# Performance work log

Measured on AMD Instinct MI355X. Metric: run time of the kernel, lower is better.

The kernel has to match this reference:

```python
import jax, jax.numpy as jnp
import numpy as np

D = 512       # d_model
M = 64        # working memory_dim
SE = 32       # episodic slots
SS = 64       # semantic slots
H = 4         # episodic heads
B, L = 2, 1024
BOT = max(D // 4, 32)  # controller bottleneck = 128


def _layernorm(x, g, b, eps=1e-5):
    mu = jnp.mean(x, axis=-1, keepdims=True)
    var = jnp.var(x, axis=-1, keepdims=True)
    return (x - mu) * jax.lax.rsqrt(var + eps) * g + b


def setup_inputs() -> dict:
    key = jax.random.key(0)
    ks = jax.random.split(key, 24)
    r = lambda i, shape, s=0.02: jax.random.normal(ks[i], shape, dtype=jnp.float32) * s
    return {
        "x": jax.random.normal(ks[0], (B, L, D), dtype=jnp.float32),
        # WorkingMemory (weights stored as (in, out))
        "Wq": r(1, (D, M)), "Wk": r(2, (D, M)), "Wv": r(3, (D, D)),
        "Wf": r(4, (D, M)), "bf": jnp.zeros((M,), jnp.float32),
        "Wo": r(5, (D, D)),
        "ln_g": jnp.ones((D,), jnp.float32), "ln_b": jnp.zeros((D,), jnp.float32),
        # EpisodicMemory
        "eslots": r(6, (1, SE, D)),
        "Eq": r(7, (D, D)), "Ek": r(8, (D, D)), "Ev": r(9, (D, D)), "Eo": r(10, (D, D)),
        # SemanticMemory
        "know": r(11, (1, SS, D)),
        "Sin": r(12, (D, D)),
        "Sg_w": r(13, (D, D)), "Sg_b": jnp.zeros((D,), jnp.float32),
        "So": r(14, (D, D)),
        # MemoryController
        "C1w": r(15, (D, BOT)), "C1b": jnp.zeros((BOT,), jnp.float32),
        "C2w": r(16, (BOT, 3)), "C2b": jnp.zeros((3,), jnp.float32),
    }


def _forward(x, Wq, Wk, Wv, Wf, bf, Wo, ln_g, ln_b,
             eslots, Eq, Ek, Ev, Eo,
             know, Sin, Sg_w, Sg_b, So,
             C1w, C1b, C2w, C2b):
    b, l, d = x.shape
    # ---- WorkingMemory (parallel gated linear attention) ----
    scale = M ** -0.5
    q = (jax.nn.elu(x @ Wq) + 1.0) * scale          # (B,L,M)
    k = jax.nn.elu(x @ Wk) + 1.0                    # (B,L,M)
    v = x @ Wv                                      # (B,L,D)
    forget = jax.nn.sigmoid(x @ Wf + bf)            # (B,L,M)
    log_f_cum = jnp.clip(jnp.cumsum(jnp.log(jnp.clip(forget, 1e-6, None)), axis=1), -20.0, 20.0)
    exp_neg = jnp.exp(-log_f_cum)
    exp_pos = jnp.exp(log_f_cum)
    kv = k[..., :, None] * v[..., None, :]          # (B,L,M,D) outer product
    cum_kv = jnp.cumsum(exp_neg[..., None] * kv, axis=1)
    Mstate = exp_pos[..., None] * cum_kv            # (B,L,M,D)
    z = exp_pos * jnp.cumsum(exp_neg * k, axis=1)   # (B,L,M)
    num = jnp.einsum('blm,blmd->bld', q, Mstate)
    den = jnp.einsum('blm,blm->bl', q, z)[..., None] + 1e-6
    w_out = _layernorm(num / den, ln_g, ln_b) @ Wo  # (B,L,D)

    # ---- EpisodicMemory (cross-attn to learned slots) ----
    hd = D // H
    mem = jnp.broadcast_to(eslots, (b, SE, D))
    qh = (x @ Eq).reshape(b, l, H, hd)
    kh = (mem @ Ek).reshape(b, SE, H, hd)
    vh = (mem @ Ev).reshape(b, SE, H, hd)
    scores = jnp.einsum('blhe,bshe->bhls', qh, kh) / jnp.sqrt(jnp.float32(hd))
    attn = jax.nn.softmax(scores, axis=-1)
    e_out = jnp.einsum('bhls,bshe->blhe', attn, vh).reshape(b, l, D) @ Eo

    # ---- SemanticMemory (single-head attn to knowledge, gated residual) ----
    kb = jnp.broadcast_to(know, (b, SS, D))
    qs = x @ Sin                                    # (B,L,D)
    s_scores = jnp.einsum('bld,bsd->bls', qs, kb) / jnp.sqrt(jnp.float32(D))
    s_attn = jax.nn.softmax(s_scores, axis=-1)
    retrieved = jnp.einsum('bls,bsd->bld', s_attn, kb)
    gate = jax.nn.sigmoid(x @ Sg_w + Sg_b)
    s_out = (gate * retrieved + (1.0 - gate) * x) @ So

    # ---- Controller fusion ----
    wts = jax.nn.softmax(jax.nn.silu(x @ C1w + C1b) @ C2w + C2b, axis=-1)  # (B,L,3)
    fused = (wts[..., 0:1] * w_out + wts[..., 1:2] * e_out + wts[..., 2:3] * s_out)
    return fused


def reference(x, Wq, Wk, Wv, Wf, bf, Wo, ln_g, ln_b,
              eslots, Eq, Ek, Ev, Eo,
              know, Sin, Sg_w, Sg_b, So,
              C1w, C1b, C2w, C2b):
    return _forward(x, Wq, Wk, Wv, Wf, bf, Wo, ln_g, ln_b,
                    eslots, Eq, Ek, Ev, Eo,
                    know, Sin, Sg_w, Sg_b, So,
                    C1w, C1b, C2w, C2b)
```

## Files before the change

kernel.cpp:

```cpp
#include <hip/hip_runtime.h>
#include <cstdint>

typedef unsigned int uint;
typedef unsigned short ushort;
typedef __attribute__((ext_vector_type(8))) short bf16x8;
typedef __attribute__((ext_vector_type(4))) float f32x4;

__device__ __forceinline__ ushort f2b(float f) {
  union { float f; uint u; } v; v.f = f;
  uint u = v.u;
  uint r = (u + 0x7FFFu + ((u >> 16) & 1u)) >> 16;
  return (ushort)r;
}
__device__ __forceinline__ float b2f(ushort h) {
  union { uint u; float f; } v; v.u = ((uint)h) << 16; return v.f;
}

__global__ __launch_bounds__(256) void k_prep(
    const float* __restrict__ x, const float* __restrict__ Wv, const float* __restrict__ Sg,
    const float* __restrict__ C1w, const float* __restrict__ Wq, const float* __restrict__ Wk,
    const float* __restrict__ Wo, const float* __restrict__ So, const float* __restrict__ know,
    const float* __restrict__ eslots, const float* __restrict__ Ek, const float* __restrict__ Ev,
    const float* __restrict__ Sin, const float* __restrict__ Wf, const float* __restrict__ bfb,
    ushort* __restrict__ X16, ushort* __restrict__ Wcat, ushort* __restrict__ Wfin,
    ushort* __restrict__ know16, float* __restrict__ kh, float* __restrict__ vh,
    float* __restrict__ logfb)
{
  __shared__ __align__(16) float Af[16 * 32];
  __shared__ __align__(16) float Bf[32 * 64];
  __shared__ __align__(16) float T[64][65];
  int bid = blockIdx.x;
  int tid = threadIdx.x;
  int lane = tid & 63, wv = tid >> 6;

  if (bid < 128) {
    int r0 = bid * 16;
    int row = tid >> 4, col4 = (tid & 15) * 4;
    float a0 = 0.f, a1 = 0.f, a2 = 0.f, a3 = 0.f;
    for (int kt = 0; kt < 16; ++kt) {
      if (tid < 128) {
        int p = tid; int rr = p >> 3, c4 = (p & 7) * 4;
        *(float4*)&Af[rr * 32 + c4] = *(const float4*)&x[(size_t)(r0 + rr) * 512 + kt * 32 + c4];
      }
      #pragma unroll
      for (int i = 0; i < 2; ++i) {
        int p = i * 256 + tid; int rr = p >> 4, c4 = (p & 15) * 4;
        *(float4*)&Bf[rr * 64 + c4] = *(const float4*)&Wf[(size_t)(kt * 32 + rr) * 64 + c4];
      }
      __syncthreads();
      #pragma unroll 8
      for (int ks = 0; ks < 32; ++ks) {
        float a = Af[row * 32 + ks];
        float4 b = *(float4*)&Bf[ks * 64 + col4];
        a0 += a * b.x; a1 += a * b.y; a2 += a * b.z; a3 += a * b.w;
      }
      __syncthreads();
    }
    float accs[4] = {a0, a1, a2, a3};
    #pragma unroll
    for (int j = 0; j < 4; ++j) {
      float logit = accs[j] + bfb[col4 + j];
      float s = 1.f / (1.f + expf(-logit));
      logfb[(size_t)(r0 + row) * 64 + col4 + j] = logf(fmaxf(s, 1e-6f));
    }
    return;
  }
  if (bid < 256) {
    int t = (bid - 128) * 256 + tid;
    if (t < 16384) {
      int s = t >> 9, j = t & 511;
      float acc = 0.f;
      #pragma unroll 8
      for (int d = 0; d < 512; ++d) acc += eslots[s * 512 + d] * Ek[d * 512 + j];
      kh[s * 512 + j] = acc;
    } else {
      int o = t - 16384; int s = o >> 9, j = o & 511;
      float acc = 0.f;
      #pragma unroll 8
      for (int d = 0; d < 512; ++d) acc += eslots[s * 512 + d] * Ev[d * 512 + j];
      vh[s * 512 + j] = acc;
    }
    return;
  }
  if (bid < 384) {
    int k = (bid - 256) * 4 + wv;
    const float* sp = Sin + (size_t)k * 512 + lane * 8;
    float4 s1 = *(const float4*)&sp[0];
    float4 s2 = *(const float4*)&sp[4];
    for (int s = 0; s < 64; ++s) {
      const float* kp = know + (size_t)s * 512 + lane * 8;
      float4 k1 = *(const float4*)&kp[0];
      float4 k2 = *(const float4*)&kp[4];
      float part = s1.x * k1.x + s1.y * k1.y + s1.z * k1.z + s1.w * k1.w
                 + s2.x * k2.x + s2.y * k2.y + s2.z * k2.z + s2.w * k2.w;
      #pragma unroll
      for (int o = 32; o; o >>= 1) part += __shfl_xor(part, o);
      if (lane == 0) Wcat[(640 + s) * 512 + k] = f2b(part * 0.04419417382415922f);
    }
    return;
  }
  if (bid < 672) {
    int tt = bid - 384;
    const float* src; ushort* dst; int sld, dld, Nt, drow, dcol;
    if (tt < 64)       {           src = Wv;  dst = Wcat; sld = 512; dld = 512;  Nt = 8; drow = 0;    dcol = 0;   }
    else if (tt < 128) { tt -= 64; src = Sg;  dst = Wcat; sld = 512; dld = 512;  Nt = 8; drow = 704;  dcol = 0;   }
    else if (tt < 144) { tt -= 128; src = C1w; dst = Wcat; sld = 128; dld = 512; Nt = 2; drow = 1216; dcol = 0;   }
    else if (tt < 152) { tt -= 144; src = Wq;  dst = Wcat; sld = 64;  dld = 512; Nt = 1; drow = 1344; dcol = 0;   }
    else if (tt < 160) { tt -= 152; src = Wk;  dst = Wcat; sld = 64;  dld = 512; Nt = 1; drow = 1408; dcol = 0;   }
    else if (tt < 224) { tt -= 160; src = Wo;  dst = Wfin; sld = 512; dld = 1152; Nt = 8; drow = 0;   dcol = 0;   }
    else               { tt -= 224; src = So;  dst = Wfin; sld = 512; dld = 1152; Nt = 8; drow = 0;   dcol = 512; }
    int tk = tt / Nt, tn = tt % Nt;
    int k0 = tk * 64, n0 = tn * 64;
    int r = tid >> 4, c = (tid & 15) * 4;
    #pragma unroll
    for (int p = 0; p < 4; ++p) {
      int kk = p * 16 + r;
      float4 v = *(const float4*)&src[(size_t)(k0 + kk) * sld + n0 + c];
      T[c + 0][kk] = v.x; T[c + 1][kk] = v.y; T[c + 2][kk] = v.z; T[c + 3][kk] = v.w;
    }
    __syncthreads();
    int n = tid >> 2, kc = (tid & 3) * 16;
    uint u[8];
    #pragma unroll
    for (int j = 0; j < 8; ++j) {
      ushort lo = f2b(T[n][kc + 2 * j]);
      ushort hi = f2b(T[n][kc + 2 * j + 1]);
      u[j] = (uint)lo | ((uint)hi << 16);
    }
    size_t off = (size_t)(drow + n0 + n) * dld + dcol + k0 + kc;
    uint4 o1; o1.x = u[0]; o1.y = u[1]; o1.z = u[2]; o1.w = u[3];
    uint4 o2; o2.x = u[4]; o2.y = u[5]; o2.z = u[6]; o2.w = u[7];
    *(uint4*)&dst[off] = o1;
    *(uint4*)&dst[off + 8] = o2;
    return;
  }
  if (bid < 800) {
    int base = (bid - 672) * 256 + tid;
    #pragma unroll
    for (int it = 0; it < 8; ++it) {
      int t = base + it * 32768;
      float4 xv = *(const float4*)&x[(size_t)t * 4];
      uint2 o;
      o.x = (uint)f2b(xv.x) | ((uint)f2b(xv.y) << 16);
      o.y = (uint)f2b(xv.z) | ((uint)f2b(xv.w) << 16);
      *(uint2*)&X16[(size_t)t * 4] = o;
    }
    return;
  }
  {
    int t = (bid - 800) * 256 + tid;
    #pragma unroll
    for (int j = 0; j < 2; ++j) {
      float4 v = *(const float4*)&know[(size_t)t * 8 + j * 4];
      uint2 o;
      o.x = (uint)f2b(v.x) | ((uint)f2b(v.y) << 16);
      o.y = (uint)f2b(v.z) | ((uint)f2b(v.w) << 16);
      *(uint2*)&know16[(size_t)t * 8 + j * 4] = o;
    }
  }
}

__global__ __launch_bounds__(256) void k_pre2(
    const float* __restrict__ Eq, const float* __restrict__ kh, const float* __restrict__ vh,
    const float* __restrict__ Eo, ushort* __restrict__ Wcat, ushort* __restrict__ Wfin)
{
  int bid = blockIdx.x;
  int tid = threadIdx.x;
  int lane = tid & 63, wv = tid >> 6;
  if (bid < 256) {
    int gw = bid * 4 + wv;
    #pragma unroll
    for (int pp = 0; pp < 2; ++pp) {
      int pair = gw * 2 + pp;
      int k = pair >> 2, h = pair & 3;
      const float* ep = Eq + (size_t)k * 512 + h * 128 + lane * 2;
      float e0 = ep[0], e1 = ep[1];
      for (int s = 0; s < 32; ++s) {
        const float* kp = kh + (size_t)s * 512 + h * 128 + lane * 2;
        float part = e0 * kp[0] + e1 * kp[1];
        #pragma unroll
        for (int o = 32; o; o >>= 1) part += __shfl_xor(part, o);
        if (lane == 0) Wcat[(512 + h * 32 + s) * 512 + k] = f2b(part * 0.08838834764831845f);
      }
    }
  } else {
    int o = (bid - 256) * 256 + tid;
    int hs = o >> 9, j = o & 511;
    int h = hs >> 5, s = hs & 31;
    const float* vhp = vh + (size_t)s * 512 + h * 128;
    float acc = 0.f;
    #pragma unroll 8
    for (int e = 0; e < 128; ++e) acc += vhp[e] * Eo[(size_t)(h * 128 + e) * 512 + j];
    Wfin[(size_t)j * 1152 + 1024 + hs] = f2b(acc);
  }
}

__global__ __launch_bounds__(256) void k_gemm1(
    const ushort* __restrict__ A, const ushort* __restrict__ Bw, float* __restrict__ C,
    const float* __restrict__ sgb, const float* __restrict__ c1b)
{
  __shared__ __align__(16) ushort As[64 * 32];
  __shared__ __align__(16) ushort Bs[128 * 32];
  int tid = threadIdx.x;
  int lane = tid & 63, wv = tid >> 6;
  int wm = (wv & 1) * 32, wn = (wv >> 1) * 64;
  int lr = lane & 15, lk = lane >> 4;
  int m0 = blockIdx.y * 64, n0 = blockIdx.x * 128;
  f32x4 zero4 = {0.f, 0.f, 0.f, 0.f};
  f32x4 acc[2][4];
  #pragma unroll
  for (int a = 0; a < 2; ++a)
    #pragma unroll
    for (int b = 0; b < 4; ++b) acc[a][b] = zero4;
  for (int kt = 0; kt < 16; ++kt) {
    int k0 = kt * 32;
    {
      int p = tid, row = p >> 2, cc = p & 3;
      int cs = cc ^ ((row >> 1) & 3);
      *(uint4*)&As[p * 8] = *(const uint4*)&A[(size_t)(m0 + row) * 512 + k0 + cs * 8];
    }
    #pragma unroll
    for (int i = 0; i < 2; ++i) {
      int p = i * 256 + tid, row = p >> 2, cc = p & 3;
      int cs = cc ^ ((row >> 1) & 3);
      *(uint4*)&Bs[p * 8] = *(const uint4*)&Bw[(size_t)(n0 + row) * 512 + k0 + cs * 8];
    }
    __syncthreads();
    bf16x8 af[2], bfv[4];
    #pragma unroll
    for (int mi = 0; mi < 2; ++mi) {
      int row = wm + mi * 16 + lr;
      int cc = lk ^ ((row >> 1) & 3);
      af[mi] = *(bf16x8*)&As[row * 32 + cc * 8];
    }
    #pragma unroll
    for (int ni = 0; ni < 4; ++ni) {
      int row = wn + ni * 16 + lr;
      int cc = lk ^ ((row >> 1) & 3);
      bfv[ni] = *(bf16x8*)&Bs[row * 32 + cc * 8];
    }
    #pragma unroll
    for (int mi = 0; mi < 2; ++mi)
      #pragma unroll
      for (int ni = 0; ni < 4; ++ni)
        acc[mi][ni] = __builtin_amdgcn_mfma_f32_16x16x32_bf16(af[mi], bfv[ni], acc[mi][ni], 0, 0, 0);
    __syncthreads();
  }
  #pragma unroll
  for (int mi = 0; mi < 2; ++mi) {
    #pragma unroll
    for (int ni = 0; ni < 4; ++ni) {
      int col = n0 + wn + ni * 16 + lr;
      #pragma unroll
      for (int r = 0; r < 4; ++r) {
        int rowb = m0 + wm + mi * 16 + lk * 4 + r;
        float v = acc[mi][ni][r];
        if (col >= 704) {
          if (col < 1216) { v = 1.f / (1.f + __expf(-(v + sgb[col - 704]))); }
          else if (col < 1344) { float tt = v + c1b[col - 1216]; v = tt / (1.f + __expf(-tt)); }
          else if (col < 1408) { float e = (v > 0.f) ? v : (__expf(v) - 1.f); v = (e + 1.f) * 0.125f; }
          else if (col < 1472) { float e = (v > 0.f) ? v : (__expf(v) - 1.f); v = e + 1.f; }
        }
        C[(size_t)rowb * 1536 + col] = v;
      }
    }
  }
}

__global__ __launch_bounds__(256) void k_gemm2(
    const ushort* __restrict__ A, const ushort* __restrict__ Bw, float* __restrict__ C)
{
  __shared__ __align__(16) ushort As[64 * 32];
  __shared__ __align__(16) ushort Bs[64 * 32];
  int tid = threadIdx.x;
  int lane = tid & 63, wv = tid >> 6;
  int wm = (wv & 1) * 32, wn = (wv >> 1) * 32;
  int lr = lane & 15, lk = lane >> 4;
  int m0 = blockIdx.y * 64, n0 = blockIdx.x * 64;
  f32x4 zero4 = {0.f, 0.f, 0.f, 0.f};
  f32x4 acc[2][2];
  #pragma unroll
  for (int a = 0; a < 2; ++a)
    #pragma unroll
    for (int b = 0; b < 2; ++b) acc[a][b] = zero4;
  for (int kt = 0; kt < 36; ++kt) {
    int k0 = kt * 32;
    {
      int p = tid, row = p >> 2, cc = p & 3;
      int cs = cc ^ ((row >> 1) & 3);
      *(uint4*)&As[p * 8] = *(const uint4*)&A[(size_t)(m0 + row) * 1152 + k0 + cs * 8];
      *(uint4*)&Bs[p * 8] = *(const uint4*)&Bw[(size_t)(n0 + row) * 1152 + k0 + cs * 8];
    }
    __syncthreads();
    bf16x8 af[2], bfv[2];
    #pragma unroll
    for (int mi = 0; mi < 2; ++mi) {
      int row = wm + mi * 16 + lr;
      int cc = lk ^ ((row >> 1) & 3);
      af[mi] = *(bf16x8*)&As[row * 32 + cc * 8];
    }
    #pragma unroll
    for (int ni = 0; ni < 2; ++ni) {
      int row = wn + ni * 16 + lr;
      int cc = lk ^ ((row >> 1) & 3);
      bfv[ni] = *(bf16x8*)&Bs[row * 32 + cc * 8];
    }
    #pragma unroll
    for (int mi = 0; mi < 2; ++mi)
      #pragma unroll
      for (int ni = 0; ni < 2; ++ni)
        acc[mi][ni] = __builtin_amdgcn_mfma_f32_16x16x32_bf16(af[mi], bfv[ni], acc[mi][ni], 0, 0, 0);
    __syncthreads();
  }
  #pragma unroll
  for (int mi = 0; mi < 2; ++mi) {
    #pragma unroll
    for (int ni = 0; ni < 2; ++ni) {
      int col = n0 + wn + ni * 16 + lr;
      #pragma unroll
      for (int r = 0; r < 4; ++r) {
        int rowb = m0 + wm + mi * 16 + lk * 4 + r;
        C[(size_t)rowb * 512 + col] = acc[mi][ni][r];
      }
    }
  }
}

__global__ __launch_bounds__(256) void k_gatescan(
    const float* __restrict__ logfb, const float* __restrict__ P,
    float* __restrict__ cn, float* __restrict__ qe, float* __restrict__ qz)
{
  __shared__ float wsumA[4];
  __shared__ float wsumB[4];
  int bidx = blockIdx.x;
  int b = bidx >> 6, m = bidx & 63;
  int tid = threadIdx.x;
  int lane = tid & 63, wv = tid >> 6;
  size_t rbase = (size_t)b * 1024 + tid * 4;

  float v0 = logfb[(rbase + 0) * 64 + m];
  float v1 = logfb[(rbase + 1) * 64 + m];
  float v2 = logfb[(rbase + 2) * 64 + m];
  float v3 = logfb[(rbase + 3) * 64 + m];
  v1 += v0; v2 += v1; v3 += v2;
  float tsum = v3;
  float sc = tsum;
  #pragma unroll
  for (int o = 1; o < 64; o <<= 1) {
    float t = __shfl_up(sc, o, 64);
    if (lane >= o) sc += t;
  }
  if (lane == 63) wsumA[wv] = sc;
  __syncthreads();
  float excl = sc - tsum;
  #pragma unroll
  for (int w2 = 0; w2 < 3; ++w2) if (w2 < wv) excl += wsumA[w2];

  float vv[4] = {v0, v1, v2, v3};
  float cv[4], qv[4];
  #pragma unroll
  for (int i = 0; i < 4; ++i) {
    size_t r = rbase + i;
    float lf = fminf(fmaxf(excl + vv[i], -20.f), 20.f);
    float en = expf(-lf), ep = expf(lf);
    float kk = P[r * 1536 + 1408 + m];
    float qq = P[r * 1536 + 1344 + m];
    cv[i] = en * kk;
    qv[i] = qq * ep;
    cn[r * 64 + m] = cv[i];
    qe[r * 64 + m] = qv[i];
  }

  float c1 = cv[0], c2 = c1 + cv[1], c3 = c2 + cv[2], c4 = c3 + cv[3];
  float t2 = c4;
  float sc2 = t2;
  #pragma unroll
  for (int o = 1; o < 64; o <<= 1) {
    float t = __shfl_up(sc2, o, 64);
    if (lane >= o) sc2 += t;
  }
  if (lane == 63) wsumB[wv] = sc2;
  __syncthreads();
  float excl2 = sc2 - t2;
  #pragma unroll
  for (int w2 = 0; w2 < 3; ++w2) if (w2 < wv) excl2 += wsumB[w2];

  float pr[4] = {c1, c2, c3, c4};
  #pragma unroll
  for (int i = 0; i < 4; ++i) {
    size_t r = rbase + i;
    qz[r * 64 + m] = qv[i] * (excl2 + pr[i]);
  }
}

__global__ __launch_bounds__(256) void k_scanA(
    const float* __restrict__ cn, const float* __restrict__ P, float* __restrict__ Send)
{
  __shared__ __align__(16) float cnS[16 * 64];
  __shared__ __align__(16) float vS[16 * 64];
  int tid = threadIdx.x;
  int bid = blockIdx.x;
  int dt = bid & 7, c = (bid >> 3) & 15, b = bid >> 7;
  int rb0 = b * 1024 + c * 64;
  int mg = tid >> 4, dl = tid & 15;
  float4 acc[4];
  #pragma unroll
  for (int i = 0; i < 4; ++i) acc[i] = make_float4(0.f, 0.f, 0.f, 0.f);
  for (int ig = 0; ig < 4; ++ig) {
    int rb = rb0 + ig * 16;
    int row = tid >> 4, c4f = (tid & 15) * 4;
    *(float4*)&cnS[row * 64 + c4f] = *(const float4*)&cn[(size_t)(rb + row) * 64 + c4f];
    *(float4*)&vS[row * 64 + c4f] = *(const float4*)&P[(size_t)(rb + row) * 1536 + dt * 64 + c4f];
    __syncthreads();
    #pragma unroll 4
    for (int i = 0; i < 16; ++i) {
      float4 vv = *(float4*)&vS[i * 64 + dl * 4];
      float4 cm = *(float4*)&cnS[i * 64 + mg * 4];
      acc[0].x += cm.x * vv.x; acc[0].y += cm.x * vv.y; acc[0].z += cm.x * vv.z; acc[0].w += cm.x * vv.w;
      acc[1].x += cm.y * vv.x; acc[1].y += cm.y * vv.y; acc[1].z += cm.y * vv.z; acc[1].w += cm.y * vv.w;
      acc[2].x += cm.z * vv.x; acc[2].y += cm.z * vv.y; acc[2].z += cm.z * vv.z; acc[2].w += cm.z * vv.w;
      acc[3].x += cm.w * vv.x; acc[3].y += cm.w * vv.y; acc[3].z += cm.w * vv.z; acc[3].w += cm.w * vv.w;
    }
    __syncthreads();
  }
  #pragma unroll
  for (int mi = 0; mi < 4; ++mi) {
    int m = mg * 4 + mi;
    *(float4*)&Send[(size_t)((b * 16 + c) * 64 + m) * 512 + dt * 64 + dl * 4] = acc[mi];
  }
}

__global__ __launch_bounds__(256) void k_scanB(const float* __restrict__ Send, float* __restrict__ carry)
{
  int t = blockIdx.x * 256 + threadIdx.x;
  int d = t & 511, m = (t >> 9) & 63, b = t >> 15;
  float run = 0.f;
  for (int c = 0; c < 16; ++c) {
    size_t idx = (size_t)((b * 16 + c) * 64 + m) * 512 + d;
    carry[idx] = run;
    run += Send[idx];
  }
}

__global__ __launch_bounds__(256) void k_scanC(
    const float* __restrict__ cn, const float* __restrict__ qe, const float* __restrict__ P,
    const float* __restrict__ carry, float* __restrict__ num)
{
  __shared__ __align__(16) float cnS[16 * 64];
  __shared__ __align__(16) float qeS[16 * 64];
  __shared__ __align__(16) float vS[16 * 64];
  int tid = threadIdx.x;
  int bid = blockIdx.x;
  int dt = bid & 7, c = (bid >> 3) & 15, b = bid >> 7;
  int rb0 = b * 1024 + c * 64;
  int mg = tid & 3, dl = tid >> 2;
  int d = dt * 64 + dl;
  float S[16];
  #pragma unroll
  for (int mi = 0; mi < 16; ++mi)
    S[mi] = carry[(size_t)((b * 16 + c) * 64 + mg * 16 + mi) * 512 + d];
  for (int ig = 0; ig < 4; ++ig) {
    int rb = rb0 + ig * 16;
    int row = tid >> 4, c4f = (tid & 15) * 4;
    *(float4*)&cnS[row * 64 + c4f] = *(const float4*)&cn[(size_t)(rb + row) * 64 + c4f];
    *(float4*)&qeS[row * 64 + c4f] = *(const float4*)&qe[(size_t)(rb + row) * 64 + c4f];
    *(float4*)&vS[row * 64 + c4f] = *(const float4*)&P[(size_t)(rb + row) * 1536 + dt * 64 + c4f];
    __syncthreads();
    for (int i = 0; i < 16; ++i) {
      float vv = vS[i * 64 + dl];
      float p = 0.f;
      #pragma unroll
      for (int j = 0; j < 4; ++j) {
        float4 c4 = *(float4*)&cnS[i * 64 + mg * 16 + j * 4];
        float4 q4 = *(float4*)&qeS[i * 64 + mg * 16 + j * 4];
        S[j * 4 + 0] += c4.x * vv; p += q4.x * S[j * 4 + 0];
        S[j * 4 + 1] += c4.y * vv; p += q4.y * S[j * 4 + 1];
        S[j * 4 + 2] += c4.z * vv; p += q4.z * S[j * 4 + 2];
        S[j * 4 + 3] += c4.w * vv; p += q4.w * S[j * 4 + 3];
      }
      p += __shfl_xor(p, 1);
      p += __shfl_xor(p, 2);
      if (mg == 0) num[(size_t)(rb + i) * 512 + d] = p;
    }
    __syncthreads();
  }
}

__global__ __launch_bounds__(256) void k_post(
    const float* __restrict__ P, const float* __restrict__ x,
    const float* __restrict__ num, const float* __restrict__ qz,
    const ushort* __restrict__ know16, const float* __restrict__ lng,
    const float* __restrict__ lnb, const float* __restrict__ C2w,
    const float* __restrict__ C2b, ushort* __restrict__ Afin)
{
  __shared__ __align__(16) ushort kbuf[32 * 512];
  __shared__ float attnL[4][64];
  __shared__ float w2L[4];
  int tid = threadIdx.x;
  int w = tid >> 6, lane = tid & 63;
  int r0 = blockIdx.x * 4;
  int r = r0 + w;
  size_t pr = (size_t)r * 1536;

  float h0 = P[pr + 1216 + lane], h1 = P[pr + 1280 + lane];
  float a0 = h0 * C2w[lane * 3 + 0] + h1 * C2w[(64 + lane) * 3 + 0];
  float a1 = h0 * C2w[lane * 3 + 1] + h1 * C2w[(64 + lane) * 3 + 1];
  float a2 = h0 * C2w[lane * 3 + 2] + h1 * C2w[(64 + lane) * 3 + 2];
  #pragma unroll
  for (int o = 32; o; o >>= 1) {
    a0 += __shfl_xor(a0, o); a1 += __shfl_xor(a1, o); a2 += __shfl_xor(a2, o);
  }
  a0 += C2b[0]; a1 += C2b[1]; a2 += C2b[2];
  float mxc = fmaxf(a0, fmaxf(a1, a2));
  float e0 = expf(a0 - mxc), e1 = expf(a1 - mxc), e2c = expf(a2 - mxc);
  float inv = 1.f / (e0 + e1 + e2c);
  float w0 = e0 * inv, w1 = e1 * inv, w2 = e2c * inv;
  if (lane == 0) w2L[w] = w2;

  {
    float den = qz[(size_t)r * 64 + lane];
    #pragma unroll
    for (int o = 32; o; o >>= 1) den += __shfl_xor(den, o);
    den += 1e-6f;
    float y[8];
    float4 n0 = *(const float4*)&num[(size_t)r * 512 + lane * 8];
    float4 n1 = *(const float4*)&num[(size_t)r * 512 + lane * 8 + 4];
    y[0] = n0.x / den; y[1] = n0.y / den; y[2] = n0.z / den; y[3] = n0.w / den;
    y[4] = n1.x / den; y[5] = n1.y / den; y[6] = n1.z / den; y[7] = n1.w / den;
    float s1 = 0.f, s2 = 0.f;
    #pragma unroll
    for (int i = 0; i < 8; ++i) { s1 += y[i]; s2 += y[i] * y[i]; }
    #pragma unroll
    for (int o = 32; o; o >>= 1) { s1 += __shfl_xor(s1, o); s2 += __shfl_xor(s2, o); }
    float mu = s1 * (1.f / 512.f);
    float var = s2 * (1.f / 512.f) - mu * mu;
    float rs = rsqrtf(var + 1e-5f);
    uint4 outv;
    uint pk[4];
    #pragma unroll
    for (int p2 = 0; p2 < 4; ++p2) {
      float o0 = (y[2 * p2] - mu) * rs * lng[lane * 8 + 2 * p2] + lnb[lane * 8 + 2 * p2];
      float o1 = (y[2 * p2 + 1] - mu) * rs * lng[lane * 8 + 2 * p2 + 1] + lnb[lane * 8 + 2 * p2 + 1];
      pk[p2] = (uint)f2b(o0 * w0) | ((uint)f2b(o1 * w0) << 16);
    }
    outv.x = pk[0]; outv.y = pk[1]; outv.z = pk[2]; outv.w = pk[3];
    *(uint4*)&Afin[(size_t)r * 1152 + lane * 8] = outv;
  }

  {
    int h = lane >> 4, ei = (lane & 15) * 2;
    float v0 = P[pr + 512 + h * 32 + ei], v1 = P[pr + 512 + h * 32 + ei + 1];
    float mxe = fmaxf(v0, v1);
    #pragma unroll
    for (int o = 1; o < 16; o <<= 1) mxe = fmaxf(mxe, __shfl_xor(mxe, o));
    float ee0 = __expf(v0 - mxe), ee1 = __expf(v1 - mxe);
    float ss = ee0 + ee1;
    #pragma unroll
    for (int o = 1; o < 16; o <<= 1) ss += __shfl_xor(ss, o);
    float sc1 = w1 / ss;
    uint pkv = (uint)f2b(ee0 * sc1) | ((uint)f2b(ee1 * sc1) << 16);
    *(uint*)&Afin[(size_t)r * 1152 + 1024 + h * 32 + ei] = pkv;
  }

  {
    float lv = P[pr + 640 + lane];
    float mx = lv;
    #pragma unroll
    for (int o = 32; o; o >>= 1) mx = fmaxf(mx, __shfl_xor(mx, o));
    float e = __expf(lv - mx);
    float sum = e;
    #pragma unroll
    for (int o = 32; o; o >>= 1) sum += __shfl_xor(sum, o);
    attnL[w][lane] = e / sum;
  }

  int dd = tid * 2;
  float acc[4][2];
  #pragma unroll
  for (int i = 0; i < 4; ++i) { acc[i][0] = 0.f; acc[i][1] = 0.f; }
  for (int hs = 0; hs < 2; ++hs) {
    #pragma unroll
    for (int i = 0; i < 8; ++i) {
      int idx = i * 256 + tid;
      *(uint4*)&kbuf[idx * 8] = *(const uint4*)&know16[(size_t)hs * 16384 + idx * 8];
    }
    __syncthreads();
    for (int s = 0; s < 32; ++s) {
      uint uu = *(uint*)&kbuf[s * 512 + dd];
      float k0 = b2f((ushort)(uu & 0xffff));
      float k1 = b2f((ushort)(uu >> 16));
      #pragma unroll
      for (int row = 0; row < 4; ++row) {
        float a = attnL[row][hs * 32 + s];
        acc[row][0] += a * k0;
        acc[row][1] += a * k1;
      }
    }
    __syncthreads();
  }
  #pragma unroll
  for (int row = 0; row < 4; ++row) {
    int rr = r0 + row;
    float g0 = P[(size_t)rr * 1536 + 704 + dd];
    float g1 = P[(size_t)rr * 1536 + 704 + dd + 1];
    float x0 = x[(size_t)rr * 512 + dd], x1 = x[(size_t)rr * 512 + dd + 1];
    float w2v = w2L[row];
    float m0 = g0 * acc[row][0] + (1.f - g0) * x0;
    float m1 = g1 * acc[row][1] + (1.f - g1) * x1;
    uint pkv = (uint)f2b(w2v * m0) | ((uint)f2b(w2v * m1) << 16);
    *(uint*)&Afin[(size_t)rr * 1152 + 512 + dd] = pkv;
  }
}

extern "C" void kernel_launch(void* const* d_in, const int* in_sizes, int n_in,
                              void* d_out, int out_size, void* d_ws, size_t ws_size,
                              hipStream_t stream)
{
  const float* x     = (const float*)d_in[0];
  const float* Wq    = (const float*)d_in[1];
  const float* Wk    = (const float*)d_in[2];
  const float* Wv    = (const float*)d_in[3];
  const float* Wf    = (const float*)d_in[4];
  const float* bfb   = (const float*)d_in[5];
  const float* Wo    = (const float*)d_in[6];
  const float* ln_g  = (const float*)d_in[7];
  const float* ln_b  = (const float*)d_in[8];
  const float* eslots= (const float*)d_in[9];
  const float* Eq    = (const float*)d_in[10];
  const float* Ek    = (const float*)d_in[11];
  const float* Ev    = (const float*)d_in[12];
  const float* Eo    = (const float*)d_in[13];
  const float* know  = (const float*)d_in[14];
  const float* Sin   = (const float*)d_in[15];
  const float* Sg_w  = (const float*)d_in[16];
  const float* Sg_b  = (const float*)d_in[17];
  const float* So    = (const float*)d_in[18];
  const float* C1w   = (const float*)d_in[19];
  const float* C1b   = (const float*)d_in[20];
  const float* C2w   = (const float*)d_in[21];
  const float* C2b   = (const float*)d_in[22];

  char* ws = (char*)d_ws;
  ushort* X16    = (ushort*)(ws + 0);
  ushort* Wcat   = (ushort*)(ws + 2097152);
  ushort* Wfin   = (ushort*)(ws + 3670016);
  ushort* know16 = (ushort*)(ws + 4849664);
  float*  kh     = (float*)(ws + 4915200);
  float*  vh     = (float*)(ws + 4980736);
  float*  P      = (float*)(ws + 5046272);
  float*  logfb  = (float*)(ws + 17629184);
  float*  cn     = (float*)(ws + 18153472);
  float*  qe     = (float*)(ws + 18677760);
  float*  qz     = (float*)(ws + 19202048);
  float*  Send   = (float*)(ws + 19726336);
  float*  carry  = (float*)(ws + 23920640);
  float*  num    = (float*)(ws + 28114944);
  ushort* Afin   = (ushort*)(ws + 32342016);

  k_prep<<<dim3(816), dim3(256), 0, stream>>>(x, Wv, Sg_w, C1w, Wq, Wk, Wo, So, know,
                                              eslots, Ek, Ev, Sin, Wf, bfb,
                                              X16, Wcat, Wfin, know16, kh, vh, logfb);
  k_pre2<<<dim3(512), dim3(256), 0, stream>>>(Eq, kh, vh, Eo, Wcat, Wfin);
  k_gemm1<<<dim3(12, 32), dim3(256), 0, stream>>>(X16, Wcat, P, Sg_b, C1b);
  k_gatescan<<<dim3(128), dim3(256), 0, stream>>>(logfb, P, cn, qe, qz);
  k_scanA<<<dim3(256), dim3(256), 0, stream>>>(cn, P, Send);
  k_scanB<<<dim3(256), dim3(256), 0, stream>>>(Send, carry);
  k_scanC<<<dim3(256), dim3(256), 0, stream>>>(cn, qe, P, carry, num);
  k_post<<<dim3(512), dim3(256), 0, stream>>>(P, x, num, qz, know16, ln_g, ln_b, C2w, C2b, Afin);
  k_gemm2<<<dim3(8, 32), dim3(256), 0, stream>>>(Afin, Wfin, (float*)d_out);
}
```

Measured before the change: 145.3 us.

## Fuse gate-scan, chunked scan passes and post-processing into one cooperative kernel

Replaces five separate launches (gatescan, scanA, scanB, scanC, post) with a single cooperative kernel of 256 blocks, using grid-wide syncs between the phases. The post phase now handles two 4-row groups per block to cover the 2048 rows. This removes four kernel launch gaps and their tail effects. In exchange it adds grid.sync overhead, leaves half the blocks idle in the first phase, and raises per-block shared memory, which may lower occupancy.

```diff
diff --git a/kernel.cpp b/kernel.cpp
--- a/kernel.cpp
+++ b/kernel.cpp
@@ -1,5 +1,8 @@
 #include <hip/hip_runtime.h>
+#include <hip/hip_cooperative_groups.h>
 #include <cstdint>
+
+namespace cg = cooperative_groups;
 
 typedef unsigned int uint;
 typedef unsigned short ushort;
@@ -326,289 +329,283 @@
   }
 }
 
-__global__ __launch_bounds__(256) void k_gatescan(
-    const float* __restrict__ logfb, const float* __restrict__ P,
-    float* __restrict__ cn, float* __restrict__ qe, float* __restrict__ qz)
+__global__ __launch_bounds__(256) void k_scanfused(
+    const float* __restrict__ P, const float* __restrict__ x, const float* __restrict__ logfb,
+    float* __restrict__ cn, float* __restrict__ qe, float* __restrict__ qz,
+    float* __restrict__ Send, float* __restrict__ carry, float* __restrict__ num,
+    const ushort* __restrict__ know16, const float* __restrict__ lng, const float* __restrict__ lnb,
+    const float* __restrict__ C2w, const float* __restrict__ C2b, ushort* __restrict__ Afin)
 {
+  cg::grid_group grid = cg::this_grid();
   __shared__ float wsumA[4];
   __shared__ float wsumB[4];
-  int bidx = blockIdx.x;
-  int b = bidx >> 6, m = bidx & 63;
-  int tid = threadIdx.x;
-  int lane = tid & 63, wv = tid >> 6;
-  size_t rbase = (size_t)b * 1024 + tid * 4;
-
-  float v0 = logfb[(rbase + 0) * 64 + m];
-  float v1 = logfb[(rbase + 1) * 64 + m];
-  float v2 = logfb[(rbase + 2) * 64 + m];
-  float v3 = logfb[(rbase + 3) * 64 + m];
-  v1 += v0; v2 += v1; v3 += v2;
-  float tsum = v3;
-  float sc = tsum;
-  #pragma unroll
-  for (int o = 1; o < 64; o <<= 1) {
-    float t = __shfl_up(sc, o, 64);
-    if (lane >= o) sc += t;
-  }
-  if (lane == 63) wsumA[wv] = sc;
-  __syncthreads();
-  float excl = sc - tsum;
-  #pragma unroll
-  for (int w2 = 0; w2 < 3; ++w2) if (w2 < wv) excl += wsumA[w2];
-
-  float vv[4] = {v0, v1, v2, v3};
-  float cv[4], qv[4];
-  #pragma unroll
-  for (int i = 0; i < 4; ++i) {
-    size_t r = rbase + i;
-    float lf = fminf(fmaxf(excl + vv[i], -20.f), 20.f);
-    float en = expf(-lf), ep = expf(lf);
-    float kk = P[r * 1536 + 1408 + m];
-    float qq = P[r * 1536 + 1344 + m];
-    cv[i] = en * kk;
-    qv[i] = qq * ep;
-    cn[r * 64 + m] = cv[i];
-    qe[r * 64 + m] = qv[i];
-  }
-
-  float c1 = cv[0], c2 = c1 + cv[1], c3 = c2 + cv[2], c4 = c3 + cv[3];
-  float t2 = c4;
-  float sc2 = t2;
-  #pragma unroll
-  for (int o = 1; o < 64; o <<= 1) {
-    float t = __shfl_up(sc2, o, 64);
-    if (lane >= o) sc2 += t;
-  }
-  if (lane == 63) wsumB[wv] = sc2;
-  __syncthreads();
-  float excl2 = sc2 - t2;
-  #pragma unroll
-  for (int w2 = 0; w2 < 3; ++w2) if (w2 < wv) excl2 += wsumB[w2];
-
-  float pr[4] = {c1, c2, c3, c4};
-  #pragma unroll
-  for (int i = 0; i < 4; ++i) {
-    size_t r = rbase + i;
-    qz[r * 64 + m] = qv[i] * (excl2 + pr[i]);
-  }
-}
-
-__global__ __launch_bounds__(256) void k_scanA(
-    const float* __restrict__ cn, const float* __restrict__ P, float* __restrict__ Send)
-{
-  __shared__ __align__(16) float cnS[16 * 64];
-  __shared__ __align__(16) float vS[16 * 64];
-  int tid = threadIdx.x;
-  int bid = blockIdx.x;
-  int dt = bid & 7, c = (bid >> 3) & 15, b = bid >> 7;
-  int rb0 = b * 1024 + c * 64;
-  int mg = tid >> 4, dl = tid & 15;
-  float4 acc[4];
-  #pragma unroll
-  for (int i = 0; i < 4; ++i) acc[i] = make_float4(0.f, 0.f, 0.f, 0.f);
-  for (int ig = 0; ig < 4; ++ig) {
-    int rb = rb0 + ig * 16;
-    int row = tid >> 4, c4f = (tid & 15) * 4;
-    *(float4*)&cnS[row * 64 + c4f] = *(const float4*)&cn[(size_t)(rb + row) * 64 + c4f];
-    *(float4*)&vS[row * 64 + c4f] = *(const float4*)&P[(size_t)(rb + row) * 1536 + dt * 64 + c4f];
-    __syncthreads();
-    #pragma unroll 4
-    for (int i = 0; i < 16; ++i) {
-      float4 vv = *(float4*)&vS[i * 64 + dl * 4];
-      float4 cm = *(float4*)&cnS[i * 64 + mg * 4];
-      acc[0].x += cm.x * vv.x; acc[0].y += cm.x * vv.y; acc[0].z += cm.x * vv.z; acc[0].w += cm.x * vv.w;
-      acc[1].x += cm.y * vv.x; acc[1].y += cm.y * vv.y; acc[1].z += cm.y * vv.z; acc[1].w += cm.y * vv.w;
-      acc[2].x += cm.z * vv.x; acc[2].y += cm.z * vv.y; acc[2].z += cm.z * vv.z; acc[2].w += cm.z * vv.w;
-      acc[3].x += cm.w * vv.x; acc[3].y += cm.w * vv.y; acc[3].z += cm.w * vv.z; acc[3].w += cm.w * vv.w;
-    }
-    __syncthreads();
-  }
-  #pragma unroll
-  for (int mi = 0; mi < 4; ++mi) {
-    int m = mg * 4 + mi;
-    *(float4*)&Send[(size_t)((b * 16 + c) * 64 + m) * 512 + dt * 64 + dl * 4] = acc[mi];
-  }
-}
-
-__global__ __launch_bounds__(256) void k_scanB(const float* __restrict__ Send, float* __restrict__ carry)
-{
-  int t = blockIdx.x * 256 + threadIdx.x;
-  int d = t & 511, m = (t >> 9) & 63, b = t >> 15;
-  float run = 0.f;
-  for (int c = 0; c < 16; ++c) {
-    size_t idx = (size_t)((b * 16 + c) * 64 + m) * 512 + d;
-    carry[idx] = run;
-    run += Send[idx];
-  }
-}
-
-__global__ __launch_bounds__(256) void k_scanC(
-    const float* __restrict__ cn, const float* __restrict__ qe, const float* __restrict__ P,
-    const float* __restrict__ carry, float* __restrict__ num)
-{
-  __shared__ __align__(16) float cnS[16 * 64];
-  __shared__ __align__(16) float qeS[16 * 64];
-  __shared__ __align__(16) float vS[16 * 64];
-  int tid = threadIdx.x;
-  int bid = blockIdx.x;
-  int dt = bid & 7, c = (bid >> 3) & 15, b = bid >> 7;
-  int rb0 = b * 1024 + c * 64;
-  int mg = tid & 3, dl = tid >> 2;
-  int d = dt * 64 + dl;
-  float S[16];
-  #pragma unroll
-  for (int mi = 0; mi < 16; ++mi)
-    S[mi] = carry[(size_t)((b * 16 + c) * 64 + mg * 16 + mi) * 512 + d];
-  for (int ig = 0; ig < 4; ++ig) {
-    int rb = rb0 + ig * 16;
-    int row = tid >> 4, c4f = (tid & 15) * 4;
-    *(float4*)&cnS[row * 64 + c4f] = *(const float4*)&cn[(size_t)(rb + row) * 64 + c4f];
-    *(float4*)&qeS[row * 64 + c4f] = *(const float4*)&qe[(size_t)(rb + row) * 64 + c4f];
-    *(float4*)&vS[row * 64 + c4f] = *(const float4*)&P[(size_t)(rb + row) * 1536 + dt * 64 + c4f];
-    __syncthreads();
-    for (int i = 0; i < 16; ++i) {
-      float vv = vS[i * 64 + dl];
-      float p = 0.f;
-      #pragma unroll
-      for (int j = 0; j < 4; ++j) {
-        float4 c4 = *(float4*)&cnS[i * 64 + mg * 16 + j * 4];
-        float4 q4 = *(float4*)&qeS[i * 64 + mg * 16 + j * 4];
-        S[j * 4 + 0] += c4.x * vv; p += q4.x * S[j * 4 + 0];
-        S[j * 4 + 1] += c4.y * vv; p += q4.y * S[j * 4 + 1];
-        S[j * 4 + 2] += c4.z * vv; p += q4.z * S[j * 4 + 2];
-        S[j * 4 + 3] += c4.w * vv; p += q4.w * S[j * 4 + 3];
-      }
-      p += __shfl_xor(p, 1);
-      p += __shfl_xor(p, 2);
-      if (mg == 0) num[(size_t)(rb + i) * 512 + d] = p;
-    }
-    __syncthreads();
-  }
-}
-
-__global__ __launch_bounds__(256) void k_post(
-    const float* __restrict__ P, const float* __restrict__ x,
-    const float* __restrict__ num, const float* __restrict__ qz,
-    const ushort* __restrict__ know16, const float* __restrict__ lng,
-    const float* __restrict__ lnb, const float* __restrict__ C2w,
-    const float* __restrict__ C2b, ushort* __restrict__ Afin)
-{
+  __shared__ __align__(16) float shA1[16 * 64];
+  __shared__ __align__(16) float shA2[16 * 64];
+  __shared__ __align__(16) float shA3[16 * 64];
   __shared__ __align__(16) ushort kbuf[32 * 512];
   __shared__ float attnL[4][64];
   __shared__ float w2L[4];
+
+  int bid = blockIdx.x;
   int tid = threadIdx.x;
-  int w = tid >> 6, lane = tid & 63;
-  int r0 = blockIdx.x * 4;
-  int r = r0 + w;
-  size_t pr = (size_t)r * 1536;
-
-  float h0 = P[pr + 1216 + lane], h1 = P[pr + 1280 + lane];
-  float a0 = h0 * C2w[lane * 3 + 0] + h1 * C2w[(64 + lane) * 3 + 0];
-  float a1 = h0 * C2w[lane * 3 + 1] + h1 * C2w[(64 + lane) * 3 + 1];
-  float a2 = h0 * C2w[lane * 3 + 2] + h1 * C2w[(64 + lane) * 3 + 2];
-  #pragma unroll
-  for (int o = 32; o; o >>= 1) {
-    a0 += __shfl_xor(a0, o); a1 += __shfl_xor(a1, o); a2 += __shfl_xor(a2, o);
-  }
-  a0 += C2b[0]; a1 += C2b[1]; a2 += C2b[2];
-  float mxc = fmaxf(a0, fmaxf(a1, a2));
-  float e0 = expf(a0 - mxc), e1 = expf(a1 - mxc), e2c = expf(a2 - mxc);
-  float inv = 1.f / (e0 + e1 + e2c);
-  float w0 = e0 * inv, w1 = e1 * inv, w2 = e2c * inv;
-  if (lane == 0) w2L[w] = w2;
+
+  if (bid < 128) {
+    int b = bid >> 6, m = bid & 63;
+    int lane = tid & 63, wvv = tid >> 6;
+    size_t rbase = (size_t)b * 1024 + tid * 4;
+    float v0 = logfb[(rbase + 0) * 64 + m];
+    float v1 = logfb[(rbase + 1) * 64 + m];
+    float v2 = logfb[(rbase + 2) * 64 + m];
+    float v3 = logfb[(rbase + 3) * 64 + m];
+    v1 += v0; v2 += v1; v3 += v2;
+    float tsum = v3;
+    float sc = tsum;
+    #pragma unroll
+    for (int o = 1; o < 64; o <<= 1) {
+      float t = __shfl_up(sc, o, 64);
+      if (lane >= o) sc += t;
+    }
+    if (lane == 63) wsumA[wvv] = sc;
+    __syncthreads();
+    float excl = sc - tsum;
+    #pragma unroll
+    for (int w2 = 0; w2 < 3; ++w2) if (w2 < wvv) excl += wsumA[w2];
+
+    float vv[4] = {v0, v1, v2, v3};
+    float cv[4], qv[4];
+    #pragma unroll
+    for (int i = 0; i < 4; ++i) {
+      size_t r = rbase + i;
+      float lf = fminf(fmaxf(excl + vv[i], -20.f), 20.f);
+      float en = expf(-lf), ep = expf(lf);
+      float kk = P[r * 1536 + 1408 + m];
+      float qq = P[r * 1536 + 1344 + m];
+      cv[i] = en * kk;
+      qv[i] = qq * ep;
+      cn[r * 64 + m] = cv[i];
+      qe[r * 64 + m] = qv[i];
+    }
+    float c1 = cv[0], c2 = c1 + cv[1], c3 = c2 + cv[2], c4 = c3 + cv[3];
+    float t2 = c4;
+    float sc2 = t2;
+    #pragma unroll
+    for (int o = 1; o < 64; o <<= 1) {
+      float t = __shfl_up(sc2, o, 64);
+      if (lane >= o) sc2 += t;
+    }
+    if (lane == 63) wsumB[wvv] = sc2;
+    __syncthreads();
+    float excl2 = sc2 - t2;
+    #pragma unroll
+    for (int w2 = 0; w2 < 3; ++w2) if (w2 < wvv) excl2 += wsumB[w2];
+    float pr[4] = {c1, c2, c3, c4};
+    #pragma unroll
+    for (int i = 0; i < 4; ++i) {
+      size_t r = rbase + i;
+      qz[r * 64 + m] = qv[i] * (excl2 + pr[i]);
+    }
+  }
+  grid.sync();
 
   {
-    float den = qz[(size_t)r * 64 + lane];
-    #pragma unroll
-    for (int o = 32; o; o >>= 1) den += __shfl_xor(den, o);
-    den += 1e-6f;
-    float y[8];
-    float4 n0 = *(const float4*)&num[(size_t)r * 512 + lane * 8];
-    float4 n1 = *(const float4*)&num[(size_t)r * 512 + lane * 8 + 4];
-    y[0] = n0.x / den; y[1] = n0.y / den; y[2] = n0.z / den; y[3] = n0.w / den;
-    y[4] = n1.x / den; y[5] = n1.y / den; y[6] = n1.z / den; y[7] = n1.w / den;
-    float s1 = 0.f, s2 = 0.f;
-    #pragma unroll
-    for (int i = 0; i < 8; ++i) { s1 += y[i]; s2 += y[i] * y[i]; }
-    #pragma unroll
-    for (int o = 32; o; o >>= 1) { s1 += __shfl_xor(s1, o); s2 += __shfl_xor(s2, o); }
-    float mu = s1 * (1.f / 512.f);
-    float var = s2 * (1.f / 512.f) - mu * mu;
-    float rs = rsqrtf(var + 1e-5f);
-    uint4 outv;
-    uint pk[4];
-    #pragma unroll
-    for (int p2 = 0; p2 < 4; ++p2) {
-      float o0 = (y[2 * p2] - mu) * rs * lng[lane * 8 + 2 * p2] + lnb[lane * 8 + 2 * p2];
-      float o1 = (y[2 * p2 + 1] - mu) * rs * lng[lane * 8 + 2 * p2 + 1] + lnb[lane * 8 + 2 * p2 + 1];
-      pk[p2] = (uint)f2b(o0 * w0) | ((uint)f2b(o1 * w0) << 16);
-    }
-    outv.x = pk[0]; outv.y = pk[1]; outv.z = pk[2]; outv.w = pk[3];
-    *(uint4*)&Afin[(size_t)r * 1152 + lane * 8] = outv;
-  }
+    float* cnS = shA1; float* vS = shA2;
+    int dt = bid & 7, c = (bid >> 3) & 15, b = bid >> 7;
+    int rb0 = b * 1024 + c * 64;
+    int mg = tid >> 4, dl = tid & 15;
+    float4 acc[4];
+    #pragma unroll
+    for (int i = 0; i < 4; ++i) acc[i] = make_float4(0.f, 0.f, 0.f, 0.f);
+    for (int ig = 0; ig < 4; ++ig) {
+      int rb = rb0 + ig * 16;
+      int row = tid >> 4, c4f = (tid & 15) * 4;
+      *(float4*)&cnS[row * 64 + c4f] = *(const float4*)&cn[(size_t)(rb + row) * 64 + c4f];
+      *(float4*)&vS[row * 64 + c4f] = *(const float4*)&P[(size_t)(rb + row) * 1536 + dt * 64 + c4f];
+      __syncthreads();
+      #pragma unroll 4
+      for (int i = 0; i < 16; ++i) {
+        float4 vv = *(float4*)&vS[i * 64 + dl * 4];
+        float4 cm = *(float4*)&cnS[i * 64 + mg * 4];
+        acc[0].x += cm.x * vv.x; acc[0].y += cm.x * vv.y; acc[0].z += cm.x * vv.z; acc[0].w += cm.x * vv.w;
+        acc[1].x += cm.y * vv.x; acc[1].y += cm.y * vv.y; acc[1].z += cm.y * vv.z; acc[1].w += cm.y * vv.w;
+        acc[2].x += cm.z * vv.x; acc[2].y += cm.z * vv.y; acc[2].z += cm.z * vv.z; acc[2].w += cm.z * vv.w;
+        acc[3].x += cm.w * vv.x; acc[3].y += cm.w * vv.y; acc[3].z += cm.w * vv.z; acc[3].w += cm.w * vv.w;
+      }
+      __syncthreads();
+    }
+    #pragma unroll
+    for (int mi = 0; mi < 4; ++mi) {
+      int m = mg * 4 + mi;
+      *(float4*)&Send[(size_t)((b * 16 + c) * 64 + m) * 512 + dt * 64 + dl * 4] = acc[mi];
+    }
+  }
+  grid.sync();
 
   {
-    int h = lane >> 4, ei = (lane & 15) * 2;
-    float v0 = P[pr + 512 + h * 32 + ei], v1 = P[pr + 512 + h * 32 + ei + 1];
-    float mxe = fmaxf(v0, v1);
-    #pragma unroll
-    for (int o = 1; o < 16; o <<= 1) mxe = fmaxf(mxe, __shfl_xor(mxe, o));
-    float ee0 = __expf(v0 - mxe), ee1 = __expf(v1 - mxe);
-    float ss = ee0 + ee1;
-    #pragma unroll
-    for (int o = 1; o < 16; o <<= 1) ss += __shfl_xor(ss, o);
-    float sc1 = w1 / ss;
-    uint pkv = (uint)f2b(ee0 * sc1) | ((uint)f2b(ee1 * sc1) << 16);
-    *(uint*)&Afin[(size_t)r * 1152 + 1024 + h * 32 + ei] = pkv;
-  }
+    int t = bid * 256 + tid;
+    int d = t & 511, m = (t >> 9) & 63, b = t >> 15;
+    float run = 0.f;
+    for (int c = 0; c < 16; ++c) {
+      size_t idx = (size_t)((b * 16 + c) * 64 + m) * 512 + d;
+      carry[idx] = run;
+      run += Send[idx];
+    }
+  }
+  grid.sync();
 
   {
-    float lv = P[pr + 640 + lane];
-    float mx = lv;
-    #pragma unroll
-    for (int o = 32; o; o >>= 1) mx = fmaxf(mx, __shfl_xor(mx, o));
-    float e = __expf(lv - mx);
-    float sum = e;
-    #pragma unroll
-    for (int o = 32; o; o >>= 1) sum += __shfl_xor(sum, o);
-    attnL[w][lane] = e / sum;
-  }
-
-  int dd = tid * 2;
-  float acc[4][2];
-  #pragma unroll
-  for (int i = 0; i < 4; ++i) { acc[i][0] = 0.f; acc[i][1] = 0.f; }
-  for (int hs = 0; hs < 2; ++hs) {
-    #pragma unroll
-    for (int i = 0; i < 8; ++i) {
-      int idx = i * 256 + tid;
-      *(uint4*)&kbuf[idx * 8] = *(const uint4*)&know16[(size_t)hs * 16384 + idx * 8];
-    }
-    __syncthreads();
-    for (int s = 0; s < 32; ++s) {
-      uint uu = *(uint*)&kbuf[s * 512 + dd];
-      float k0 = b2f((ushort)(uu & 0xffff));
-      float k1 = b2f((ushort)(uu >> 16));
-      #pragma unroll
-      for (int row = 0; row < 4; ++row) {
-        float a = attnL[row][hs * 32 + s];
-        acc[row][0] += a * k0;
-        acc[row][1] += a * k1;
-      }
-    }
-    __syncthreads();
-  }
-  #pragma unroll
-  for (int row = 0; row < 4; ++row) {
-    int rr = r0 + row;
-    float g0 = P[(size_t)rr * 1536 + 704 + dd];
-    float g1 = P[(size_t)rr * 1536 + 704 + dd + 1];
-    float x0 = x[(size_t)rr * 512 + dd], x1 = x[(size_t)rr * 512 + dd + 1];
-    float w2v = w2L[row];
-    float m0 = g0 * acc[row][0] + (1.f - g0) * x0;
-    float m1 = g1 * acc[row][1] + (1.f - g1) * x1;
-    uint pkv = (uint)f2b(w2v * m0) | ((uint)f2b(w2v * m1) << 16);
-    *(uint*)&Afin[(size_t)rr * 1152 + 512 + dd] = pkv;
+    float* cnS = shA1; float* qeS = shA2; float* vS = shA3;
+    int dt = bid & 7, c = (bid >> 3) & 15, b = bid >> 7;
+    int rb0 = b * 1024 + c * 64;
+    int mg = tid & 3, dl = tid >> 2;
+    int d = dt * 64 + dl;
+    float S[16];
+    #pragma unroll
+    for (int mi = 0; mi < 16; ++mi)
+      S[mi] = carry[(size_t)((b * 16 + c) * 64 + mg * 16 + mi) * 512 + d];
+    for (int ig = 0; ig < 4; ++ig) {
+      int rb = rb0 + ig * 16;
+      int row = tid >> 4, c4f = (tid & 15) * 4;
+      *(float4*)&cnS[row * 64 + c4f] = *(const float4*)&cn[(size_t)(rb + row) * 64 + c4f];
+      *(float4*)&qeS[row * 64 + c4f] = *(const float4*)&qe[(size_t)(rb + row) * 64 + c4f];
+      *(float4*)&vS[row * 64 + c4f] = *(const float4*)&P[(size_t)(rb + row) * 1536 + dt * 64 + c4f];
+      __syncthreads();
+      for (int i = 0; i < 16; ++i) {
+        float vv = vS[i * 64 + dl];
+        float p = 0.f;
+        #pragma unroll
+        for (int j = 0; j < 4; ++j) {
+          float4 c4 = *(float4*)&cnS[i * 64 + mg * 16 + j * 4];
+          float4 q4 = *(float4*)&qeS[i * 64 + mg * 16 + j * 4];
+          S[j * 4 + 0] += c4.x * vv; p += q4.x * S[j * 4 + 0];
+          S[j * 4 + 1] += c4.y * vv; p += q4.y * S[j * 4 + 1];
+          S[j * 4 + 2] += c4.z * vv; p += q4.z * S[j * 4 + 2];
+          S[j * 4 + 3] += c4.w * vv; p += q4.w * S[j * 4 + 3];
+        }
+        p += __shfl_xor(p, 1);
+        p += __shfl_xor(p, 2);
+        if (mg == 0) num[(size_t)(rb + i) * 512 + d] = p;
+      }
+      __syncthreads();
+    }
+  }
+  grid.sync();
+
+  for (int g = 0; g < 2; ++g) {
+    __syncthreads();
+    int w = tid >> 6, lane = tid & 63;
+    int r0 = (bid * 2 + g) * 4;
+    int r = r0 + w;
+    size_t pr = (size_t)r * 1536;
+
+    float h0 = P[pr + 1216 + lane], h1 = P[pr + 1280 + lane];
+    float a0 = h0 * C2w[lane * 3 + 0] + h1 * C2w[(64 + lane) * 3 + 0];
+    float a1 = h0 * C2w[lane * 3 + 1] + h1 * C2w[(64 + lane) * 3 + 1];
+    float a2 = h0 * C2w[lane * 3 + 2] + h1 * C2w[(64 + lane) * 3 + 2];
+    #pragma unroll
+    for (int o = 32; o; o >>= 1) {
+      a0 += __shfl_xor(a0, o); a1 += __shfl_xor(a1, o); a2 += __shfl_xor(a2, o);
+    }
+    a0 += C2b[0]; a1 += C2b[1]; a2 += C2b[2];
+    float mxc = fmaxf(a0, fmaxf(a1, a2));
+    float e0 = expf(a0 - mxc), e1 = expf(a1 - mxc), e2c = expf(a2 - mxc);
+    float inv = 1.f / (e0 + e1 + e2c);
+    float w0 = e0 * inv, w1 = e1 * inv, w2 = e2c * inv;
+    if (lane == 0) w2L[w] = w2;
+
+    {
+      float den = qz[(size_t)r * 64 + lane];
+      #pragma unroll
+      for (int o = 32; o; o >>= 1) den += __shfl_xor(den, o);
+      den += 1e-6f;
+      float y[8];
+      float4 n0 = *(const float4*)&num[(size_t)r * 512 + lane * 8];
+      float4 n1 = *(const float4*)&num[(size_t)r * 512 + lane * 8 + 4];
+      y[0] = n0.x / den; y[1] = n0.y / den; y[2] = n0.z / den; y[3] = n0.w / den;
+      y[4] = n1.x / den; y[5] = n1.y / den; y[6] = n1.z / den; y[7] = n1.w / den;
+      float s1 = 0.f, s2 = 0.f;
+      #pragma unroll
+      for (int i = 0; i < 8; ++i) { s1 += y[i]; s2 += y[i] * y[i]; }
+      #pragma unroll
+      for (int o = 32; o; o >>= 1) { s1 += __shfl_xor(s1, o); s2 += __shfl_xor(s2, o); }
+      float mu = s1 * (1.f / 512.f);
+      float var = s2 * (1.f / 512.f) - mu * mu;
+      float rs = rsqrtf(var + 1e-5f);
+      uint4 outv;
+      uint pk[4];
+      #pragma unroll
+      for (int p2 = 0; p2 < 4; ++p2) {
+        float o0 = (y[2 * p2] - mu) * rs * lng[lane * 8 + 2 * p2] + lnb[lane * 8 + 2 * p2];
+        float o1 = (y[2 * p2 + 1] - mu) * rs * lng[lane * 8 + 2 * p2 + 1] + lnb[lane * 8 + 2 * p2 + 1];
+        pk[p2] = (uint)f2b(o0 * w0) | ((uint)f2b(o1 * w0) << 16);
+      }
+      outv.x = pk[0]; outv.y = pk[1]; outv.z = pk[2]; outv.w = pk[3];
+      *(uint4*)&Afin[(size_t)r * 1152 + lane * 8] = outv;
+    }
+
+    {
+      int h = lane >> 4, ei = (lane & 15) * 2;
+      float v0 = P[pr + 512 + h * 32 + ei], v1 = P[pr + 512 + h * 32 + ei + 1];
+      float mxe = fmaxf(v0, v1);
+      #pragma unroll
+      for (int o = 1; o < 16; o <<= 1) mxe = fmaxf(mxe, __shfl_xor(mxe, o));
+      float ee0 = __expf(v0 - mxe), ee1 = __expf(v1 - mxe);
+      float ss = ee0 + ee1;
+      #pragma unroll
+      for (int o = 1; o < 16; o <<= 1) ss += __shfl_xor(ss, o);
+      float sc1 = w1 / ss;
+      uint pkv = (uint)f2b(ee0 * sc1) | ((uint)f2b(ee1 * sc1) << 16);
+      *(uint*)&Afin[(size_t)r * 1152 + 1024 + h * 32 + ei] = pkv;
+    }
+
+    {
+      float lv = P[pr + 640 + lane];
+      float mx = lv;
+      #pragma unroll
+      for (int o = 32; o; o >>= 1) mx = fmaxf(mx, __shfl_xor(mx, o));
+      float e = __expf(lv - mx);
+      float sum = e;
+      #pragma unroll
+      for (int o = 32; o; o >>= 1) sum += __shfl_xor(sum, o);
+      attnL[w][lane] = e / sum;
+    }
+    __syncthreads();
+
+    int dd = tid * 2;
+    float acc[4][2];
+    #pragma unroll
+    for (int i = 0; i < 4; ++i) { acc[i][0] = 0.f; acc[i][1] = 0.f; }
+    for (int hs = 0; hs < 2; ++hs) {
+      #pragma unroll
+      for (int i = 0; i < 8; ++i) {
+        int idx = i * 256 + tid;
+        *(uint4*)&kbuf[idx * 8] = *(const uint4*)&know16[(size_t)hs * 16384 + idx * 8];
+      }
+      __syncthreads();
+      for (int s = 0; s < 32; ++s) {
+        uint uu = *(uint*)&kbuf[s * 512 + dd];
+        float k0 = b2f((ushort)(uu & 0xffff));
+        float k1 = b2f((ushort)(uu >> 16));
+        #pragma unroll
+        for (int row = 0; row < 4; ++row) {
+          float a = attnL[row][hs * 32 + s];
+          acc[row][0] += a * k0;
+          acc[row][1] += a * k1;
+        }
+      }
+      __syncthreads();
+    }
+    #pragma unroll
+    for (int row = 0; row < 4; ++row) {
+      int rr = r0 + row;
+      float g0 = P[(size_t)rr * 1536 + 704 + dd];
+      float g1 = P[(size_t)rr * 1536 + 704 + dd + 1];
+      float x0 = x[(size_t)rr * 512 + dd], x1 = x[(size_t)rr * 512 + dd + 1];
+      float w2v = w2L[row];
+      float m0 = g0 * acc[row][0] + (1.f - g0) * x0;
+      float m1 = g1 * acc[row][1] + (1.f - g1) * x1;
+      uint pkv = (uint)f2b(w2v * m0) | ((uint)f2b(w2v * m1) << 16);
+      *(uint*)&Afin[(size_t)rr * 1152 + 512 + dd] = pkv;
+    }
   }
 }
 
@@ -662,10 +659,11 @@
                                               X16, Wcat, Wfin, know16, kh, vh, logfb);
   k_pre2<<<dim3(512), dim3(256), 0, stream>>>(Eq, kh, vh, Eo, Wcat, Wfin);
   k_gemm1<<<dim3(12, 32), dim3(256), 0, stream>>>(X16, Wcat, P, Sg_b, C1b);
-  k_gatescan<<<dim3(128), dim3(256), 0, stream>>>(logfb, P, cn, qe, qz);
-  k_scanA<<<dim3(256), dim3(256), 0, stream>>>(cn, P, Send);
-  k_scanB<<<dim3(256), dim3(256), 0, stream>>>(Send, carry);
-  k_scanC<<<dim3(256), dim3(256), 0, stream>>>(cn, qe, P, carry, num);
-  k_post<<<dim3(512), dim3(256), 0, stream>>>(P, x, num, qz, know16, ln_g, ln_b, C2w, C2b, Afin);
+
+  void* args[] = { (void*)&P, (void*)&x, (void*)&logfb, (void*)&cn, (void*)&qe, (void*)&qz,
+                   (void*)&Send, (void*)&carry, (void*)&num, (void*)&know16,
+                   (void*)&ln_g, (void*)&ln_b, (void*)&C2w, (void*)&C2b, (void*)&Afin };
+  hipLaunchCooperativeKernel((const void*)k_scanfused, dim3(256), dim3(256), args, 0, stream);
+
   k_gemm2<<<dim3(8, 32), dim3(256), 0, stream>>>(Afin, Wfin, (float*)d_out);
 }
```

Result: slower. 282.6 us (+94.5%).
